# Kernel optimization log

Measured on AMD Instinct MI355X. Metric: run time of the kernel, lower is better.

Reference implementation:

```python
import jax, jax.numpy as jnp
import numpy as np

N = 8192          # total samples = n_ways * num_instances
D = 512           # embedding dim
NUM_INSTANCES = 8 # shots per class
MARGIN = 0.3
W = 1.0
EPS = 1e-12


def setup_inputs() -> dict:
    key = jax.random.key(0)
    inputs = jax.random.normal(key, (N, D), dtype=jnp.float32)
    # targets[i] = class id; classes are contiguous blocks of NUM_INSTANCES
    targets = jnp.arange(N, dtype=jnp.int32) // NUM_INSTANCES
    return {"inputs": inputs, "targets": targets}


def _pairwise_euclid(a, b):
    # sqrt(clamp(||a||^2 + ||b||^2 - 2 a.b, eps)) -- same as torch addmm path
    sq_a = jnp.sum(a * a, axis=1)          # [na]
    sq_b = jnp.sum(b * b, axis=1)          # [nb]
    d2 = sq_a[:, None] + sq_b[None, :] - 2.0 * (a @ b.T)
    return jnp.sqrt(jnp.clip(d2, EPS, None))


def reference(inputs, targets):
    n = inputs.shape[0]
    n_ways = n // NUM_INSTANCES

    dist = _pairwise_euclid(inputs, inputs)              # [n, n]
    mask = targets[:, None] == targets[None, :]          # same-class mask

    # batch-hard mining: hardest positive (max same-class dist),
    # hardest negative (min different-class dist), fully vectorized
    dist_ap = jnp.max(jnp.where(mask, dist, -jnp.inf), axis=1)  # [n]
    dist_an = jnp.min(jnp.where(mask, jnp.inf, dist), axis=1)   # [n]

    # MarginRankingLoss with y=1: mean(relu(-(dist_an - dist_ap) + margin))
    loss = jnp.mean(jax.nn.relu(dist_ap - dist_an + MARGIN))

    dist_p = jnp.mean(dist_ap)
    dist_n = jnp.mean(dist_an)

    # prototype accuracy
    protos = inputs.reshape(n_ways, NUM_INSTANCES, -1).mean(axis=1)  # [n_ways, D]
    logits = _pairwise_euclid(inputs, protos)                        # [n, n_ways]
    estimate = jnp.argmin(logits, axis=1)
    labels = jnp.arange(n_ways, dtype=estimate.dtype).repeat(NUM_INSTANCES)
    acc = jnp.mean((estimate == labels).astype(jnp.float32))

    return (W * loss, acc, dist_p, dist_n)
```

## Files before the change

kernel.cpp:

```cpp
#include <hip/hip_runtime.h>
#include <hip/hip_bf16.h>
#include <stdint.h>

#define NTOT  8192
#define DIM   512
#define NI    8
#define NWAYS 1024
#define TILE  128
#define BK    128
#define NSYM  2080
#define NBLK  2592
#define MARGINV 0.3f

typedef float f32x4 __attribute__((ext_vector_type(4)));

__device__ __forceinline__ unsigned f2o(float f) {
  unsigned u = __float_as_uint(f);
  return (u & 0x80000000u) ? ~u : (u | 0x80000000u);
}
__device__ __forceinline__ float o2f(unsigned u) {
  u = (u & 0x80000000u) ? (u & 0x7fffffffu) : ~u;
  return __uint_as_float(u);
}

__device__ __forceinline__ float wave_sum64(float v) {
#pragma unroll
  for (int s = 32; s; s >>= 1) v += __shfl_xor(v, s, 64);
  return v;
}

__device__ __forceinline__ void async_ld16(const void* g, void* l) {
  __builtin_amdgcn_global_load_lds(
      (__attribute__((address_space(1))) void*)(uintptr_t)g,
      (__attribute__((address_space(3))) void*)l, 16, 0, 0);
}

__global__ __launch_bounds__(256) void prep(
    const float* __restrict__ A, float* __restrict__ sq,
    float* __restrict__ psq, unsigned char* __restrict__ A8,
    unsigned char* __restrict__ P8,
    unsigned* __restrict__ an_u32, unsigned* __restrict__ ap_u32,
    unsigned long long* __restrict__ pr_key) {
  const int w = threadIdx.x >> 6;
  const int l = threadIdx.x & 63;
  const int b = blockIdx.x;
  if (b < NTOT / 4) {
    const int row = b * 4 + w;
    const float4* rp = (const float4*)(A + (size_t)row * DIM);
    unsigned* op = (unsigned*)(A8 + (size_t)row * DIM);
    float s = 0.f;
#pragma unroll
    for (int m = 0; m < 2; ++m) {
      const float4 v = rp[l + 64 * m];
      s = fmaf(v.x, v.x, fmaf(v.y, v.y, fmaf(v.z, v.z, fmaf(v.w, v.w, s))));
      int wd = 0;
      wd = __builtin_amdgcn_cvt_pk_fp8_f32(v.x, v.y, wd, false);
      wd = __builtin_amdgcn_cvt_pk_fp8_f32(v.z, v.w, wd, true);
      op[l + 64 * m] = (unsigned)wd;
    }
    s = wave_sum64(s);
    if (l == 0) {
      sq[row] = s;
      an_u32[row] = ~0u;
      ap_u32[row] = 0u;
      pr_key[row] = ~0ull;
    }
  } else {
    const int c = (b - NTOT / 4) * 4 + w;
    unsigned* op = (unsigned*)(P8 + (size_t)c * DIM);
    float s = 0.f;
#pragma unroll
    for (int m = 0; m < 2; ++m) {
      float4 p = {0.f, 0.f, 0.f, 0.f};
#pragma unroll
      for (int r = 0; r < NI; ++r) {
        const float4 v =
            ((const float4*)(A + (size_t)(c * NI + r) * DIM))[l + 64 * m];
        p.x += v.x; p.y += v.y; p.z += v.z; p.w += v.w;
      }
      p.x *= (1.f / NI); p.y *= (1.f / NI); p.z *= (1.f / NI); p.w *= (1.f / NI);
      s = fmaf(p.x, p.x, fmaf(p.y, p.y, fmaf(p.z, p.z, fmaf(p.w, p.w, s))));
      int wd = 0;
      wd = __builtin_amdgcn_cvt_pk_fp8_f32(p.x, p.y, wd, false);
      wd = __builtin_amdgcn_cvt_pk_fp8_f32(p.z, p.w, wd, true);
      op[l + 64 * m] = (unsigned)wd;
    }
    s = wave_sum64(s);
    if (l == 0) psq[c] = s;
  }
}

__global__ __launch_bounds__(256) void gemm_fused(
    const unsigned char* __restrict__ A, const unsigned char* __restrict__ P,
    const float* __restrict__ sq, const float* __restrict__ psq,
    unsigned* __restrict__ an_u32, unsigned* __restrict__ ap_u32,
    unsigned long long* __restrict__ pr_key) {
  __shared__ __align__(16) unsigned char As[2][TILE * BK];
  __shared__ __align__(16) unsigned char Bs[2][TILE * BK];
  __shared__ unsigned rmin[TILE];
  __shared__ unsigned cmin[TILE];
  __shared__ unsigned amax[TILE];
  __shared__ unsigned long long rowkey[TILE][2];

  const int braw = blockIdx.x;
  const int b = (braw & 7) * (NBLK / 8) + (braw >> 3);
  const bool isProto = b >= NSYM;
  int bi, bj;
  const unsigned char* Bmat;
  const float* sqB;
  if (!isProto) {
    int rem = b, Si = 0, Sj = 0;
    for (;;) {
      const int cnt = (Si == Sj) ? 36 : 64;
      if (rem < cnt) break;
      rem -= cnt;
      ++Si;
      if (Si > Sj) { Si = 0; ++Sj; }
    }
    int bi_l, bj_l;
    if (Si == Sj) {
      bj_l = 0;
      while ((bj_l + 1) * (bj_l + 2) / 2 <= rem) ++bj_l;
      bi_l = rem - bj_l * (bj_l + 1) / 2;
    } else {
      bi_l = rem & 7;
      bj_l = rem >> 3;
    }
    bi = Si * 8 + bi_l;
    bj = Sj * 8 + bj_l;
    Bmat = A;
    sqB = sq;
  } else {
    const int p = b - NSYM;
    bj = p & 7;
    bi = p >> 3;
    Bmat = P;
    sqB = psq;
  }
  const int rowBase = bi * TILE;
  const int colBase = bj * TILE;
  const bool isDiag = !isProto && (bi == bj);
  const bool colSide = !isProto && (bi != bj);

  const int t = threadIdx.x;
  const int lane = t & 63;
  const int wv = t >> 6;
  const int wr = wv >> 1;
  const int wc = wv & 1;
  const int quad = lane >> 4;
  const int lc = lane & 15;

  if (t < TILE) { rmin[t] = ~0u; cmin[t] = ~0u; amax[t] = 0u; }

  int koff[4];
#pragma unroll
  for (int c = 0; c < 4; ++c)
    koff[c] = (((c * 2 + (quad >> 1)) ^ (lc & 7)) * 16) + (quad & 1) * 8;

  int rowA[4], rowB[4];
#pragma unroll
  for (int x = 0; x < 4; ++x) {
    rowA[x] = (wr * 64 + x * 16 + lc) * BK;
    rowB[x] = (wc * 64 + x * 16 + lc) * BK;
  }

  const int l8 = lane >> 3;
  const int ul = ((lane & 7) ^ (l8 & 7)) * 16;
  const unsigned char* gA = A + (size_t)(rowBase + l8) * DIM + ul;
  const unsigned char* gB = Bmat + (size_t)(colBase + l8) * DIM + ul;
  const int ldsL = lane * 16;

  f32x4 acc[4][4] = {};

#pragma unroll
  for (int j = 0; j < 4; ++j) {
    const int rr = wv * 4 + j;
    async_ld16(gA + (size_t)rr * 8 * DIM, &As[0][rr * 1024 + ldsL]);
    async_ld16(gB + (size_t)rr * 8 * DIM, &Bs[0][rr * 1024 + ldsL]);
  }
  __syncthreads();

#pragma unroll
  for (int it = 0; it < 4; ++it) {
    const int cur = it & 1;
    const int nxt = cur ^ 1;
    const int kt = it * BK;
    if (it < 3) {
#pragma unroll
      for (int j = 0; j < 4; ++j) {
        const int rr = wv * 4 + j;
        async_ld16(gA + (size_t)rr * 8 * DIM + kt + BK, &As[nxt][rr * 1024 + ldsL]);
        async_ld16(gB + (size_t)rr * 8 * DIM + kt + BK, &Bs[nxt][rr * 1024 + ldsL]);
      }
    }
    const unsigned char* Ac = &As[cur][0];
    const unsigned char* Bc = &Bs[cur][0];
#pragma unroll
    for (int c = 0; c < 4; ++c) {
      long af[4], bfr[4];
#pragma unroll
      for (int x = 0; x < 4; ++x) {
        af[x]  = *(const long*)(Ac + rowA[x] + koff[c]);
        bfr[x] = *(const long*)(Bc + rowB[x] + koff[c]);
      }
#pragma unroll
      for (int x = 0; x < 4; ++x)
#pragma unroll
        for (int y = 0; y < 4; ++y)
          acc[x][y] = __builtin_amdgcn_mfma_f32_16x16x32_fp8_fp8(
              af[x], bfr[y], acc[x][y], 0, 0, 0);
    }
    __syncthreads();
  }

  float sb[4];
#pragma unroll
  for (int y = 0; y < 4; ++y) sb[y] = sqB[colBase + wc * 64 + y * 16 + lc];

  const float INF = __int_as_float(0x7f800000);

  if (!isProto) {
#pragma unroll
    for (int x = 0; x < 4; ++x) {
#pragma unroll
      for (int r = 0; r < 4; ++r) {
        const int row = rowBase + wr * 64 + x * 16 + quad * 4 + r;
        float mv = INF, mx = -INF;
#pragma unroll
        for (int y = 0; y < 4; ++y) {
          const float v = fmaf(-2.f, acc[x][y][r], sb[y]);
          if (isDiag) {
            const int col = colBase + wc * 64 + y * 16 + lc;
            const bool same = (row >> 3) == (col >> 3);
            mv = fminf(mv, same ? INF : v);
            mx = fmaxf(mx, same ? v : -INF);
          } else {
            mv = fminf(mv, v);
          }
        }
        atomicMin(&rmin[row - rowBase], f2o(mv));
        if (isDiag) atomicMax(&amax[row - rowBase], f2o(mx));
      }
    }
    if (colSide) {
      float sa[4][4];
#pragma unroll
      for (int x = 0; x < 4; ++x)
#pragma unroll
        for (int r = 0; r < 4; ++r)
          sa[x][r] = sq[rowBase + wr * 64 + x * 16 + quad * 4 + r];
#pragma unroll
      for (int y = 0; y < 4; ++y) {
        float cv = INF;
#pragma unroll
        for (int x = 0; x < 4; ++x)
#pragma unroll
          for (int r = 0; r < 4; ++r)
            cv = fminf(cv, fmaf(-2.f, acc[x][y][r], sa[x][r]));
        atomicMin(&cmin[wc * 64 + y * 16 + lc], f2o(cv));
      }
    }
  } else {
#pragma unroll
    for (int x = 0; x < 4; ++x) {
      unsigned long long kmin[4] = {~0ull, ~0ull, ~0ull, ~0ull};
#pragma unroll
      for (int y = 0; y < 4; ++y) {
        const int col = colBase + wc * 64 + y * 16 + lc;
#pragma unroll
        for (int r = 0; r < 4; ++r) {
          const float v = fmaf(-2.f, acc[x][y][r], sb[y]);
          const unsigned long long kn =
              ((unsigned long long)f2o(v) << 32) | (unsigned)col;
          if (kn < kmin[r]) kmin[r] = kn;
        }
      }
#pragma unroll
      for (int r = 0; r < 4; ++r) {
#pragma unroll
        for (int s = 1; s < 16; s <<= 1) {
          const unsigned long long o = __shfl_xor(kmin[r], s, 64);
          if (o < kmin[r]) kmin[r] = o;
        }
      }
      if (lc == 0) {
#pragma unroll
        for (int r = 0; r < 4; ++r)
          rowkey[wr * 64 + x * 16 + quad * 4 + r][wc] = kmin[r];
      }
    }
  }

  __syncthreads();
  if (isProto) {
    if (t < TILE) {
      unsigned long long a = rowkey[t][0];
      const unsigned long long c = rowkey[t][1];
      if (c < a) a = c;
      atomicMin(pr_key + rowBase + t, a);
    }
  } else {
    if (t < TILE) {
      atomicMin(an_u32 + rowBase + t, rmin[t]);
    } else if (t < 2 * TILE) {
      const int i = t - TILE;
      if (colSide) atomicMin(an_u32 + colBase + i, cmin[i]);
      else if (isDiag) atomicMax(ap_u32 + rowBase + i, amax[i]);
    }
  }
}

__global__ void finalize_kernel(const float* __restrict__ sq,
                                const unsigned* __restrict__ an_u32,
                                const unsigned* __restrict__ ap_u32,
                                const unsigned long long* __restrict__ pr_key,
                                float* __restrict__ out) {
  const int tid = threadIdx.x;
  float loss = 0.f, sp = 0.f, sn = 0.f, acc = 0.f;
#pragma unroll
  for (int i = tid; i < NTOT; i += 1024) {
    const float s = sq[i];
    const float ap = sqrtf(fmaxf(s + o2f(ap_u32[i]), 1e-12f));
    const float an = sqrtf(fmaxf(s + o2f(an_u32[i]), 1e-12f));
    loss += fmaxf(ap - an + MARGINV, 0.f);
    sp += ap;
    sn += an;
    acc += ((unsigned)(pr_key[i] & 0xffffffffu) == (unsigned)(i >> 3)) ? 1.f : 0.f;
  }
  loss = wave_sum64(loss);
  sp = wave_sum64(sp);
  sn = wave_sum64(sn);
  acc = wave_sum64(acc);
  __shared__ float red[16][4];
  const int w = tid >> 6, l = tid & 63;
  if (l == 0) { red[w][0] = loss; red[w][1] = acc; red[w][2] = sp; red[w][3] = sn; }
  __syncthreads();
  if (tid == 0) {
    float L = 0, Ac = 0, Pm = 0, Nn = 0;
    for (int i = 0; i < 16; ++i) {
      L += red[i][0]; Ac += red[i][1]; Pm += red[i][2]; Nn += red[i][3];
    }
    out[0] = L / NTOT;
    out[1] = Ac / NTOT;
    out[2] = Pm / NTOT;
    out[3] = Nn / NTOT;
  }
}

extern "C" void kernel_launch(void* const* d_in, const int* in_sizes, int n_in,
                              void* d_out, int out_size, void* d_ws, size_t ws_size,
                              hipStream_t stream) {
  const float* inputs = (const float*)d_in[0];
  float* out = (float*)d_out;
  char* w = (char*)d_ws;
  float* sq  = (float*)(w);
  float* psq = (float*)(w + 32768);
  unsigned* an_u32 = (unsigned*)(w + 36864);
  unsigned* ap_u32 = (unsigned*)(w + 69632);
  unsigned long long* pr_key = (unsigned long long*)(w + 102400);
  unsigned char* A8 = (unsigned char*)(w + 167936);
  unsigned char* P8 = (unsigned char*)(w + 167936 + (size_t)NTOT * DIM);

  prep<<<NTOT / 4 + NWAYS / 4, 256, 0, stream>>>(inputs, sq, psq, A8, P8,
                                                 an_u32, ap_u32, pr_key);
  gemm_fused<<<NBLK, 256, 0, stream>>>(A8, P8, sq, psq,
                                       an_u32, ap_u32, pr_key);
  finalize_kernel<<<1, 1024, 0, stream>>>(sq, an_u32, ap_u32, pr_key, out);
}
```

Before: 135.0 us.

## Load GEMM fragments directly from global memory and reduce epilogue with shuffles

Removes the LDS double-buffered async staging of FP8 tiles. Each wave now loads its MFMA operand fragments straight from global memory into registers, with a two-deep register prefetch across 16 K-chunks. The epilogue replaces shared-memory atomics with wave shuffle reductions that write per-wave partials to LDS, and launch bounds now ask for 4 blocks per CU. This cuts LDS traffic, barriers and LDS usage to raise occupancy. The cost is uncoalesced 8-byte global loads with operands re-read across waves, which depends on L1/L2 absorbing the reuse.

```diff
diff --git a/kernel.cpp b/kernel.cpp
--- a/kernel.cpp
+++ b/kernel.cpp
@@ -7,7 +7,6 @@
 #define NI    8
 #define NWAYS 1024
 #define TILE  128
-#define BK    128
 #define NSYM  2080
 #define NBLK  2592
 #define MARGINV 0.3f
@@ -27,12 +26,6 @@
 #pragma unroll
   for (int s = 32; s; s >>= 1) v += __shfl_xor(v, s, 64);
   return v;
-}
-
-__device__ __forceinline__ void async_ld16(const void* g, void* l) {
-  __builtin_amdgcn_global_load_lds(
-      (__attribute__((address_space(1))) void*)(uintptr_t)g,
-      (__attribute__((address_space(3))) void*)l, 16, 0, 0);
 }
 
 __global__ __launch_bounds__(256) void prep(
@@ -90,16 +83,14 @@
   }
 }
 
-__global__ __launch_bounds__(256) void gemm_fused(
+__global__ __launch_bounds__(256, 4) void gemm_fused(
     const unsigned char* __restrict__ A, const unsigned char* __restrict__ P,
     const float* __restrict__ sq, const float* __restrict__ psq,
     unsigned* __restrict__ an_u32, unsigned* __restrict__ ap_u32,
     unsigned long long* __restrict__ pr_key) {
-  __shared__ __align__(16) unsigned char As[2][TILE * BK];
-  __shared__ __align__(16) unsigned char Bs[2][TILE * BK];
-  __shared__ unsigned rmin[TILE];
-  __shared__ unsigned cmin[TILE];
-  __shared__ unsigned amax[TILE];
+  __shared__ float rminL[TILE][2];
+  __shared__ float cminL[TILE][2];
+  __shared__ float amaxL[TILE][2];
   __shared__ unsigned long long rowkey[TILE][2];
 
   const int braw = blockIdx.x;
@@ -150,67 +141,39 @@
   const int quad = lane >> 4;
   const int lc = lane & 15;
 
-  if (t < TILE) { rmin[t] = ~0u; cmin[t] = ~0u; amax[t] = 0u; }
-
-  int koff[4];
-#pragma unroll
-  for (int c = 0; c < 4; ++c)
-    koff[c] = (((c * 2 + (quad >> 1)) ^ (lc & 7)) * 16) + (quad & 1) * 8;
-
-  int rowA[4], rowB[4];
+  const unsigned char* pA[4];
+  const unsigned char* pB[4];
 #pragma unroll
   for (int x = 0; x < 4; ++x) {
-    rowA[x] = (wr * 64 + x * 16 + lc) * BK;
-    rowB[x] = (wc * 64 + x * 16 + lc) * BK;
-  }
-
-  const int l8 = lane >> 3;
-  const int ul = ((lane & 7) ^ (l8 & 7)) * 16;
-  const unsigned char* gA = A + (size_t)(rowBase + l8) * DIM + ul;
-  const unsigned char* gB = Bmat + (size_t)(colBase + l8) * DIM + ul;
-  const int ldsL = lane * 16;
+    pA[x] = A + (size_t)(rowBase + wr * 64 + x * 16 + lc) * DIM + quad * 8;
+    pB[x] = Bmat + (size_t)(colBase + wc * 64 + x * 16 + lc) * DIM + quad * 8;
+  }
 
   f32x4 acc[4][4] = {};
-
-#pragma unroll
-  for (int j = 0; j < 4; ++j) {
-    const int rr = wv * 4 + j;
-    async_ld16(gA + (size_t)rr * 8 * DIM, &As[0][rr * 1024 + ldsL]);
-    async_ld16(gB + (size_t)rr * 8 * DIM, &Bs[0][rr * 1024 + ldsL]);
-  }
-  __syncthreads();
-
-#pragma unroll
-  for (int it = 0; it < 4; ++it) {
-    const int cur = it & 1;
-    const int nxt = cur ^ 1;
-    const int kt = it * BK;
-    if (it < 3) {
-#pragma unroll
-      for (int j = 0; j < 4; ++j) {
-        const int rr = wv * 4 + j;
-        async_ld16(gA + (size_t)rr * 8 * DIM + kt + BK, &As[nxt][rr * 1024 + ldsL]);
-        async_ld16(gB + (size_t)rr * 8 * DIM + kt + BK, &Bs[nxt][rr * 1024 + ldsL]);
-      }
-    }
-    const unsigned char* Ac = &As[cur][0];
-    const unsigned char* Bc = &Bs[cur][0];
-#pragma unroll
-    for (int c = 0; c < 4; ++c) {
-      long af[4], bfr[4];
+  long af[2][4], bf[2][4];
+
+#pragma unroll
+  for (int x = 0; x < 4; ++x) {
+    af[0][x] = *(const long*)(pA[x]);
+    bf[0][x] = *(const long*)(pB[x]);
+  }
+#pragma unroll
+  for (int ch = 0; ch < 16; ++ch) {
+    const int cur = ch & 1, nxt = cur ^ 1;
+    if (ch < 15) {
+      const int ko = (ch + 1) * 32;
 #pragma unroll
       for (int x = 0; x < 4; ++x) {
-        af[x]  = *(const long*)(Ac + rowA[x] + koff[c]);
-        bfr[x] = *(const long*)(Bc + rowB[x] + koff[c]);
-      }
-#pragma unroll
-      for (int x = 0; x < 4; ++x)
-#pragma unroll
-        for (int y = 0; y < 4; ++y)
-          acc[x][y] = __builtin_amdgcn_mfma_f32_16x16x32_fp8_fp8(
-              af[x], bfr[y], acc[x][y], 0, 0, 0);
-    }
-    __syncthreads();
+        af[nxt][x] = *(const long*)(pA[x] + ko);
+        bf[nxt][x] = *(const long*)(pB[x] + ko);
+      }
+    }
+#pragma unroll
+    for (int x = 0; x < 4; ++x)
+#pragma unroll
+      for (int y = 0; y < 4; ++y)
+        acc[x][y] = __builtin_amdgcn_mfma_f32_16x16x32_fp8_fp8(
+            af[cur][x], bf[cur][y], acc[x][y], 0, 0, 0);
   }
 
   float sb[4];
@@ -224,22 +187,30 @@
     for (int x = 0; x < 4; ++x) {
 #pragma unroll
       for (int r = 0; r < 4; ++r) {
-        const int row = rowBase + wr * 64 + x * 16 + quad * 4 + r;
+        const int rloc = wr * 64 + x * 16 + quad * 4 + r;
         float mv = INF, mx = -INF;
 #pragma unroll
         for (int y = 0; y < 4; ++y) {
           const float v = fmaf(-2.f, acc[x][y][r], sb[y]);
           if (isDiag) {
             const int col = colBase + wc * 64 + y * 16 + lc;
-            const bool same = (row >> 3) == (col >> 3);
+            const bool same = ((rowBase + rloc) >> 3) == (col >> 3);
             mv = fminf(mv, same ? INF : v);
             mx = fmaxf(mx, same ? v : -INF);
           } else {
             mv = fminf(mv, v);
           }
         }
-        atomicMin(&rmin[row - rowBase], f2o(mv));
-        if (isDiag) atomicMax(&amax[row - rowBase], f2o(mx));
+#pragma unroll
+        for (int s = 1; s < 16; s <<= 1) mv = fminf(mv, __shfl_xor(mv, s, 64));
+        if (isDiag) {
+#pragma unroll
+          for (int s = 1; s < 16; s <<= 1) mx = fmaxf(mx, __shfl_xor(mx, s, 64));
+        }
+        if (lc == 0) {
+          rminL[rloc][wc] = mv;
+          if (isDiag) amaxL[rloc][wc] = mx;
+        }
       }
     }
     if (colSide) {
@@ -257,7 +228,9 @@
 #pragma unroll
           for (int r = 0; r < 4; ++r)
             cv = fminf(cv, fmaf(-2.f, acc[x][y][r], sa[x][r]));
-        atomicMin(&cmin[wc * 64 + y * 16 + lc], f2o(cv));
+#pragma unroll
+        for (int s = 16; s < 64; s <<= 1) cv = fminf(cv, __shfl_xor(cv, s, 64));
+        if (quad == 0) cminL[wc * 64 + y * 16 + lc][wr] = cv;
       }
     }
   } else {
@@ -301,11 +274,13 @@
     }
   } else {
     if (t < TILE) {
-      atomicMin(an_u32 + rowBase + t, rmin[t]);
+      atomicMin(an_u32 + rowBase + t, f2o(fminf(rminL[t][0], rminL[t][1])));
     } else if (t < 2 * TILE) {
       const int i = t - TILE;
-      if (colSide) atomicMin(an_u32 + colBase + i, cmin[i]);
-      else if (isDiag) atomicMax(ap_u32 + rowBase + i, amax[i]);
+      if (colSide)
+        atomicMin(an_u32 + colBase + i, f2o(fminf(cminL[i][0], cminL[i][1])));
+      else if (isDiag)
+        atomicMax(ap_u32 + rowBase + i, f2o(fmaxf(amaxL[i][0], amaxL[i][1])));
     }
   }
 }
```

New measurement: 245.2 us. +81.6%, slower.
